# Performance work log

Hardware: AMD Instinct MI355X
Metric: run time of the kernel (lower is better)

The kernel has to match this reference:

```python
import jax, jax.numpy as jnp
import numpy as np
from jax import lax

TAU = 2.0
VTH = 1.0
EPS = 1e-5


def heaviside(x):
    return (x >= 0.0).astype(x.dtype)


def lif_scan(x):
    """x: [T, ...]; LIF with decay_input=True, v_reset=0 (hard reset)."""
    def step(v, xt):
        v = v + (xt - v) / TAU
        s = heaviside(v - VTH)
        v = v * (1.0 - s)
        return v, s
    _, out = lax.scan(step, jnp.zeros_like(x[0]), x)
    return out


def conv2d(x, w):
    return lax.conv_general_dilated(x, w, (1, 1), 'SAME',
                                    dimension_numbers=('NCHW', 'OIHW', 'NCHW'))


def bn(x, g, b, m, v):
    inv = lax.rsqrt(v + EPS)
    return (x - m[None, :, None, None]) * (g * inv)[None, :, None, None] + b[None, :, None, None]


def maxpool2(x):
    return lax.reduce_window(x, -jnp.inf, lax.max, (1, 1, 2, 2), (1, 1, 2, 2), 'VALID')


def conv_block(x, w, g, b, m, v, pool):
    T, B = x.shape[:2]
    y = x.reshape((T * B,) + x.shape[2:])
    y = bn(conv2d(y, w), g, b, m, v)
    y = y.reshape((T, B) + y.shape[1:])
    y = lif_scan(y)
    if pool:
        y = y.reshape((T * B,) + y.shape[2:])
        y = maxpool2(y)
        y = y.reshape((T, B) + y.shape[1:])
    return y


def setup_inputs() -> dict:
    key = jax.random.key(0)
    ks = jax.random.split(key, 12)
    x = jax.random.normal(ks[0], (8, 128, 3, 32, 32), jnp.float32)
    w1 = jax.random.normal(ks[1], (64, 3, 3, 3), jnp.float32) * 0.1
    w2 = jax.random.normal(ks[2], (128, 64, 3, 3), jnp.float32) * 0.05
    w3 = jax.random.normal(ks[3], (256, 128, 3, 3), jnp.float32) * 0.05
    fc1_w = jax.random.normal(ks[4], (512, 16384), jnp.float32) * 0.01
    raw = jax.random.normal(ks[5], (10, 512), jnp.float32)
    Q, _ = jnp.linalg.qr(raw.T)  # 10 <= 512: orthogonal prototypes
    protos = Q.T[:10]
    d = dict(x=x, w1=w1, w2=w2, w3=w3, fc1_w=fc1_w, protos=protos)
    for i, c in zip((1, 2, 3), (64, 128, 256)):
        d[f'g{i}'] = jnp.ones((c,), jnp.float32)
        d[f'b{i}'] = jnp.zeros((c,), jnp.float32)
        d[f'm{i}'] = jax.random.normal(jax.random.fold_in(key, 100 + i), (c,), jnp.float32) * 0.1
        d[f'var{i}'] = jax.random.uniform(jax.random.fold_in(key, 200 + i), (c,), jnp.float32) + 0.5
    return d


def reference(x, w1, g1, b1, m1, var1, w2, g2, b2, m2, var2,
              w3, g3, b3, m3, var3, fc1_w, protos):
    h = conv_block(x, w1, g1, b1, m1, var1, pool=False)   # [T,B,64,32,32]
    h = conv_block(h, w2, g2, b2, m2, var2, pool=True)    # [T,B,128,16,16]
    h = conv_block(h, w3, g3, b3, m3, var3, pool=True)    # [T,B,256,8,8]
    T, B = h.shape[:2]
    h = h.reshape(T, B, -1)                               # [T,B,16384]
    h = jnp.einsum('tbd,fd->tbf', h, fc1_w)
    h = lif_scan(h)                                        # [T,B,512]
    feat = h.mean(axis=0)                                  # [B,512]
    fn = feat / jnp.clip(jnp.linalg.norm(feat, axis=1, keepdims=True), 1e-12)
    pn = protos / jnp.clip(jnp.linalg.norm(protos, axis=1, keepdims=True), 1e-12)
    return fn @ pn.T * 10.0                                # [B,10]
```

## Files before the change

kernel.cpp:

```cpp
#include <hip/hip_runtime.h>
#include <stdint.h>

#define EPS 1e-5f

typedef __attribute__((ext_vector_type(4))) float f32x4;
typedef __attribute__((ext_vector_type(8))) __bf16 bf16x8;

__device__ __forceinline__ void gl_lds16(const void* g, void* l) {
    __builtin_amdgcn_global_load_lds(
        (const __attribute__((address_space(1))) void*)g,
        (__attribute__((address_space(3))) void*)l, 16, 0, 0);
}

__device__ __forceinline__ unsigned short f2bf(float f) {
    unsigned u = __builtin_bit_cast(unsigned, f);
    unsigned r = (u + 0x7FFFu + ((u >> 16) & 1u)) >> 16;
    return (unsigned short)r;
}
__device__ __forceinline__ float bf2f(unsigned short h) {
    unsigned u = ((unsigned)h) << 16;
    return __builtin_bit_cast(float, u);
}

#define OFF_W2S   0ULL
#define OFF_W3S   442368ULL
#define OFF_FCS   2211840ULL
#define OFF_S1M   52543488ULL
#define OFF_S2PM  60932096ULL
#define OFF_S3    65126400ULL
#define OFF_PRE4P 98680832ULL
#define OFF_FEAT  115458048ULL
#define OFF_PN    115720192ULL

__global__ void repack_w2s(const float* __restrict__ w2, unsigned short* __restrict__ out) {
    int i = blockIdx.x * 256 + threadIdx.x;
    if (i >= 73728) return;
    int oc = i / 576, rem = i % 576;
    int ic = rem / 9, tap = rem % 9;
    float w = w2[i];
    unsigned short hi = f2bf(w);  float r1 = w - bf2f(hi);
    unsigned short md = f2bf(r1); float r2 = r1 - bf2f(md);
    unsigned short lo = f2bf(r2);
    size_t base = ((size_t)(tap * 128 + oc)) * 64 + (((ic >> 3) ^ (oc & 7)) << 3) + (ic & 7);
    out[base] = hi; out[base + 73728] = md; out[base + 147456] = lo;
}
__global__ void repack_w3s(const float* __restrict__ w3, unsigned short* __restrict__ out) {
    int i = blockIdx.x * 256 + threadIdx.x;
    if (i >= 294912) return;
    int oc = i / 1152, rem = i % 1152;
    int ic = rem / 9, tap = rem % 9;
    float w = w3[i];
    unsigned short hi = f2bf(w);  float r1 = w - bf2f(hi);
    unsigned short md = f2bf(r1); float r2 = r1 - bf2f(md);
    unsigned short lo = f2bf(r2);
    int cc = tap * 2 + (ic >> 6), icl = ic & 63;
    size_t base = ((size_t)(cc * 256 + oc)) * 64 + (((icl >> 3) ^ (oc & 7)) << 3) + (icl & 7);
    out[base] = hi; out[base + 294912] = md; out[base + 589824] = lo;
}
__global__ void repack_fcs(const float* __restrict__ fw, unsigned short* __restrict__ out) {
    int i = blockIdx.x * 256 + threadIdx.x;
    if (i >= 8388608) return;
    int f = i >> 14, d = i & 16383;
    float w = fw[i];
    unsigned short hi = f2bf(w);  float r1 = w - bf2f(hi);
    unsigned short md = f2bf(r1); float r2 = r1 - bf2f(md);
    unsigned short lo = f2bf(r2);
    int cc = d >> 6, kl = d & 63;
    size_t base = (((size_t)cc << 9) + f) * 64 + (((kl >> 3) ^ (f & 7)) << 3) + (kl & 7);
    out[base] = hi; out[base + 8388608] = md; out[base + 16777216] = lo;
}

__global__ __launch_bounds__(256) void conv1_lif_pack(
    const float* __restrict__ x, const float* __restrict__ w1,
    const float* __restrict__ g1, const float* __restrict__ b1,
    const float* __restrict__ m1, const float* __restrict__ var1,
    unsigned long long* __restrict__ s1m)
{
    __shared__ float xt[3][3][40];
    int blk = blockIdx.x;
    int b = blk >> 5, y = blk & 31;
    int tid = threadIdx.x;
    int w = tid >> 6, lane = tid & 63;

    float wr[27];
#pragma unroll
    for (int j = 0; j < 27; ++j) wr[j] = w1[lane * 27 + j];
    float scale = g1[lane] / sqrtf(var1[lane] + EPS);
    float bias  = b1[lane] - m1[lane] * scale;

    float v[8];
#pragma unroll
    for (int p = 0; p < 8; ++p) v[p] = 0.f;

    for (int t = 0; t < 8; ++t) {
        __syncthreads();
        const float* xb = x + ((size_t)(t * 128 + b)) * 3072;
        for (int i = tid; i < 360; i += 256) {
            int ic = i / 120, rem = i % 120, dr = rem / 40, col = rem % 40;
            int yy = y + dr - 1, xx = col - 4;
            float val = 0.f;
            if (yy >= 0 && yy < 32 && xx >= 0 && xx < 32)
                val = xb[ic * 1024 + yy * 32 + xx];
            xt[ic][dr][col] = val;
        }
        __syncthreads();

        float acc[8];
#pragma unroll
        for (int p = 0; p < 8; ++p) acc[p] = 0.f;
#pragma unroll
        for (int ic = 0; ic < 3; ++ic)
#pragma unroll
        for (int dr = 0; dr < 3; ++dr) {
            const float* row = &xt[ic][dr][w * 8];
            float bf[16];
            *(float4*)&bf[0]  = *(const float4*)&row[0];
            *(float4*)&bf[4]  = *(const float4*)&row[4];
            *(float4*)&bf[8]  = *(const float4*)&row[8];
            *(float4*)&bf[12] = *(const float4*)&row[12];
#pragma unroll
            for (int p = 0; p < 8; ++p)
#pragma unroll
                for (int dxm = 0; dxm < 3; ++dxm)
                    acc[p] += bf[p + dxm + 3] * wr[ic * 9 + dr * 3 + dxm];
        }
        size_t base = ((size_t)t * 128 + b) * 1024 + y * 32 + w * 8;
#pragma unroll
        for (int p = 0; p < 8; ++p) {
            float pre = acc[p] * scale + bias;
            v[p] = v[p] + (pre - v[p]) * 0.5f;
            bool s = (v[p] >= 1.0f);
            unsigned long long mk = __ballot(s);
            if (s) v[p] = 0.f;
            if (lane == 0) s1m[base + p] = mk;
        }
    }
}

__global__ __launch_bounds__(256, 2) void conv2_mfma(
    const unsigned long long* __restrict__ s1m,
    const unsigned short* __restrict__ w2s,
    const float* __restrict__ g, const float* __restrict__ bb,
    const float* __restrict__ mm, const float* __restrict__ vv,
    unsigned long long* __restrict__ s2pm)
{
    __shared__ unsigned short A[128 * 64];
    __shared__ unsigned short B[3 * 128 * 64];
    __shared__ unsigned long long mt[6][34];
    __shared__ unsigned short pm16[2][16][8];

    int tid = threadIdx.x;
    int m0 = blockIdx.x << 7;
    int b = m0 >> 10;
    int pix0 = m0 & 1023;
    int y0 = pix0 >> 5;

    int w = tid >> 6, lane = tid & 63;
    int wm = w & 1, wn = w >> 1;
    int q = lane >> 4, r = lane & 15;
    int swr = r & 7;
    int am = tid >> 1, ah = tid & 1;
    int ay = am >> 5, ax = am & 31;
    int asw = am & 7;

    float scl[4], bia[4];
#pragma unroll
    for (int j = 0; j < 4; ++j) {
        int oc = wn * 64 + j * 16 + r;
        float s0 = g[oc] / sqrtf(vv[oc] + EPS);
        scl[j] = s0;
        bia[j] = bb[oc] - mm[oc] * s0;
    }

    float vr[4][4][4];
#pragma unroll
    for (int i = 0; i < 4; ++i)
#pragma unroll
        for (int j = 0; j < 4; ++j)
#pragma unroll
            for (int k = 0; k < 4; ++k) vr[i][j][k] = 0.f;

    const char* w2sb = (const char*)w2s;

    for (int t = 0; t < 8; ++t) {
        for (int i = tid; i < 204; i += 256) {
            int ly = i / 34, lx = i % 34;
            int yy = y0 + ly - 1, xx = lx - 1;
            unsigned long long mv = 0ULL;
            if (yy >= 0 && yy < 32 && xx >= 0 && xx < 32)
                mv = s1m[(size_t)t * 131072 + (b << 10) + (yy << 5) + xx];
            mt[ly][lx] = mv;
        }

        f32x4 acc[4][4];
#pragma unroll
        for (int i = 0; i < 4; ++i)
#pragma unroll
            for (int j = 0; j < 4; ++j) acc[i][j] = (f32x4){0.f, 0.f, 0.f, 0.f};

        for (int tap = 0; tap < 9; ++tap) {
            int dy = tap / 3, dx = tap - dy * 3;
            __syncthreads();
            {
                unsigned long long mk = mt[ay + dy][ax + dx];
                unsigned int wbits = (unsigned int)(mk >> (ah << 5));
#pragma unroll
                for (int c4 = 0; c4 < 4; ++c4) {
                    unsigned int bt = wbits >> (c4 << 3);
                    uint4 val;
                    val.x = ((bt & 1u) ? 0x3F80u : 0u)  | ((bt & 2u) ? 0x3F800000u : 0u);
                    val.y = ((bt & 4u) ? 0x3F80u : 0u)  | ((bt & 8u) ? 0x3F800000u : 0u);
                    val.z = ((bt & 16u) ? 0x3F80u : 0u) | ((bt & 32u) ? 0x3F800000u : 0u);
                    val.w = ((bt & 64u) ? 0x3F80u : 0u) | ((bt & 128u) ? 0x3F800000u : 0u);
                    int c = (ah << 2) + c4;
                    *(uint4*)((char*)A + am * 128 + ((c ^ asw) << 4)) = val;
                }
            }
            {
                const char* gb = w2sb + tap * 16384 + (w << 12) + (lane << 4);
                char* lb = (char*)B + (w << 12);
#pragma unroll
                for (int s = 0; s < 3; ++s)
#pragma unroll
                    for (int p = 0; p < 4; ++p)
                        gl_lds16(gb + s * 147456 + (p << 10), lb + s * 16384 + (p << 10));
            }
            __syncthreads();
#pragma unroll
            for (int ks = 0; ks < 2; ++ks) {
                bf16x8 af[4];
#pragma unroll
                for (int i = 0; i < 4; ++i)
                    af[i] = *(const bf16x8*)((const char*)A + (wm * 64 + i * 16 + r) * 128 + ((((ks << 2) + q) ^ swr) << 4));
#pragma unroll
                for (int s = 0; s < 3; ++s) {
                    bf16x8 bfr[4];
#pragma unroll
                    for (int j = 0; j < 4; ++j)
                        bfr[j] = *(const bf16x8*)((const char*)B + s * 16384 + (wn * 64 + j * 16 + r) * 128 + ((((ks << 2) + q) ^ swr) << 4));
#pragma unroll
                    for (int i = 0; i < 4; ++i)
#pragma unroll
                        for (int j = 0; j < 4; ++j)
                            acc[i][j] = __builtin_amdgcn_mfma_f32_16x16x32_bf16(af[i], bfr[j], acc[i][j], 0, 0, 0);
                }
            }
        }

        unsigned long long S = 0ULL;
#pragma unroll
        for (int i = 0; i < 4; ++i) {
#pragma unroll
            for (int j = 0; j < 4; ++j) {
#pragma unroll
                for (int reg = 0; reg < 4; ++reg) {
                    float pre = acc[i][j][reg] * scl[j] + bia[j];
                    float vo = vr[i][j][reg];
                    vo = vo + (pre - vo) * 0.5f;
                    bool sp = (vo >= 1.0f);
                    vr[i][j][reg] = sp ? 0.f : vo;
                    if (sp) S |= 1ULL << (i * 16 + j * 4 + reg);
                }
            }
        }
#pragma unroll
        for (int b1 = 0; b1 < 2; ++b1)
#pragma unroll
            for (int u = 0; u < 2; ++u)
#pragma unroll
                for (int j = 0; j < 4; ++j) {
                    int k0 = b1 * 16 + j * 4 + 2 * u;
                    bool sp = (((S >> k0) | (S >> (k0 + 1)) | (S >> (k0 + 32)) | (S >> (k0 + 33))) & 1ULL) != 0;
                    unsigned long long mk = __ballot(sp);
                    if (r == 0)
                        pm16[wm][b1 * 8 + (q << 1) + u][wn * 4 + j] = (unsigned short)(mk >> (q << 4));
                }
        __syncthreads();
        if (tid < 64) {
            int py = tid >> 5, px = (tid >> 1) & 15, h = tid & 1;
            unsigned long long vmk = *(unsigned long long*)&pm16[py][px][h << 2];
            s2pm[(size_t)t * 65536 + ((size_t)(b << 8) + ((y0 >> 1) + py) * 16 + px) * 2 + h] = vmk;
        }
    }
}

__global__ __launch_bounds__(256, 2) void conv3_mfma(
    const unsigned long long* __restrict__ s2pm,
    const unsigned short* __restrict__ w3s,
    const float* __restrict__ g, const float* __restrict__ bb,
    const float* __restrict__ mm, const float* __restrict__ vv,
    unsigned short* __restrict__ s3)
{
    __shared__ unsigned short A[128 * 64];
    __shared__ unsigned short B[3 * 128 * 64];
    __shared__ unsigned long long mt3[10][18][2];

    int tid = threadIdx.x;
    int m0 = blockIdx.x << 7;
    int n0 = blockIdx.y << 7;
    int b = m0 >> 8;
    int pix0 = m0 & 255;
    int y0 = pix0 >> 4;

    int w = tid >> 6, lane = tid & 63;
    int wm = w & 1, wn = w >> 1;
    int q = lane >> 4, r = lane & 15;
    int swr = r & 7;
    int am = tid >> 1, ah = tid & 1;
    int ay = am >> 4, ax = am & 15;
    int asw = am & 7;

    float scl[4], bia[4];
#pragma unroll
    for (int j = 0; j < 4; ++j) {
        int oc = n0 + wn * 64 + j * 16 + r;
        float s0 = g[oc] / sqrtf(vv[oc] + EPS);
        scl[j] = s0;
        bia[j] = bb[oc] - mm[oc] * s0;
    }

    float vr[4][4][4];
#pragma unroll
    for (int i = 0; i < 4; ++i)
#pragma unroll
        for (int j = 0; j < 4; ++j)
#pragma unroll
            for (int k = 0; k < 4; ++k) vr[i][j][k] = 0.f;

    const char* w3sb = (const char*)w3s;
    int bsw = b & 7;

    for (int t = 0; t < 8; ++t) {
        for (int i = tid; i < 180; i += 256) {
            int ly = i / 18, lx = i % 18;
            int yy = y0 + ly - 1, xx = lx - 1;
            unsigned long long v0 = 0ULL, v1 = 0ULL;
            if (yy >= 0 && yy < 16 && xx >= 0 && xx < 16) {
                const unsigned long long* p = &s2pm[(size_t)t * 65536 + ((size_t)(b << 8) + (yy << 4) + xx) * 2];
                v0 = p[0]; v1 = p[1];
            }
            mt3[ly][lx][0] = v0; mt3[ly][lx][1] = v1;
        }

        f32x4 acc[4][4];
#pragma unroll
        for (int i = 0; i < 4; ++i)
#pragma unroll
            for (int j = 0; j < 4; ++j) acc[i][j] = (f32x4){0.f, 0.f, 0.f, 0.f};

        for (int cc = 0; cc < 18; ++cc) {
            int tap = cc >> 1, h = cc & 1;
            int dy = tap / 3, dx = tap - dy * 3;
            __syncthreads();
            {
                unsigned long long mk = mt3[ay + dy][ax + dx][h];
                unsigned int wbits = (unsigned int)(mk >> (ah << 5));
#pragma unroll
                for (int c4 = 0; c4 < 4; ++c4) {
                    unsigned int bt = wbits >> (c4 << 3);
                    uint4 val;
                    val.x = ((bt & 1u) ? 0x3F80u : 0u)  | ((bt & 2u) ? 0x3F800000u : 0u);
                    val.y = ((bt & 4u) ? 0x3F80u : 0u)  | ((bt & 8u) ? 0x3F800000u : 0u);
                    val.z = ((bt & 16u) ? 0x3F80u : 0u) | ((bt & 32u) ? 0x3F800000u : 0u);
                    val.w = ((bt & 64u) ? 0x3F80u : 0u) | ((bt & 128u) ? 0x3F800000u : 0u);
                    int c = (ah << 2) + c4;
                    *(uint4*)((char*)A + am * 128 + ((c ^ asw) << 4)) = val;
                }
            }
            {
                const char* gb = w3sb + cc * 32768 + n0 * 128 + (w << 12) + (lane << 4);
                char* lb = (char*)B + (w << 12);
#pragma unroll
                for (int s = 0; s < 3; ++s)
#pragma unroll
                    for (int p = 0; p < 4; ++p)
                        gl_lds16(gb + s * 589824 + (p << 10), lb + s * 16384 + (p << 10));
            }
            __syncthreads();
#pragma unroll
            for (int ks = 0; ks < 2; ++ks) {
                bf16x8 af[4];
#pragma unroll
                for (int i = 0; i < 4; ++i)
                    af[i] = *(const bf16x8*)((const char*)A + (wm * 64 + i * 16 + r) * 128 + ((((ks << 2) + q) ^ swr) << 4));
#pragma unroll
                for (int s = 0; s < 3; ++s) {
                    bf16x8 bfr[4];
#pragma unroll
                    for (int j = 0; j < 4; ++j)
                        bfr[j] = *(const bf16x8*)((const char*)B + s * 16384 + (wn * 64 + j * 16 + r) * 128 + ((((ks << 2) + q) ^ swr) << 4));
#pragma unroll
                    for (int i = 0; i < 4; ++i)
#pragma unroll
                        for (int j = 0; j < 4; ++j)
                            acc[i][j] = __builtin_amdgcn_mfma_f32_16x16x32_bf16(af[i], bfr[j], acc[i][j], 0, 0, 0);
                }
            }
        }

        unsigned long long S = 0ULL;
#pragma unroll
        for (int i = 0; i < 4; ++i) {
#pragma unroll
            for (int j = 0; j < 4; ++j) {
#pragma unroll
                for (int reg = 0; reg < 4; ++reg) {
                    float pre = acc[i][j][reg] * scl[j] + bia[j];
                    float vo = vr[i][j][reg];
                    vo = vo + (pre - vo) * 0.5f;
                    bool sp = (vo >= 1.0f);
                    vr[i][j][reg] = sp ? 0.f : vo;
                    if (sp) S |= 1ULL << (i * 16 + j * 4 + reg);
                }
            }
        }
        unsigned short* s3t = s3 + (size_t)t * 2097152;
#pragma unroll
        for (int a2 = 0; a2 < 2; ++a2)
#pragma unroll
            for (int u = 0; u < 2; ++u)
#pragma unroll
                for (int j = 0; j < 4; ++j) {
                    int kA = 32 * a2 + j * 4 + 2 * u;
                    bool sp = (((S >> kA) | (S >> (kA + 1)) | (S >> (kA + 16)) | (S >> (kA + 17))) & 1ULL) != 0;
                    int oc = n0 + wn * 64 + j * 16 + r;
                    int y2 = (y0 >> 1) + wm * 2 + a2;
                    int x2 = (q << 1) + u;
                    s3t[(size_t)(b << 14) + oc * 64 + ((y2 ^ bsw) << 3) + x2] =
                        (unsigned short)(sp ? 0x3F80 : 0);
                }
    }
}

__global__ __launch_bounds__(256, 2) void fc_mfma(
    const unsigned short* __restrict__ s3,
    const unsigned short* __restrict__ fcs,
    float* __restrict__ pre4p)
{
    __shared__ unsigned short A[128 * 64];
    __shared__ unsigned short B[3 * 128 * 64];

    int tid = threadIdx.x;
    int m0 = blockIdx.x << 7;
    int n0 = blockIdx.y << 7;
    int kseg = blockIdx.z;
    int cc0 = kseg << 5;

    int w = tid >> 6, lane = tid & 63;
    int wm = w & 1, wn = w >> 1;
    int q = lane >> 4, r = lane & 15;
    int swr = r & 7;

    f32x4 acc[4][4];
#pragma unroll
    for (int i = 0; i < 4; ++i)
#pragma unroll
        for (int j = 0; j < 4; ++j) acc[i][j] = (f32x4){0.f, 0.f, 0.f, 0.f};

    const char* s3b = (const char*)s3;
    const char* fcsb = (const char*)fcs;

    for (int cc = cc0; cc < cc0 + 32; ++cc) {
        __syncthreads();
        {
            char* lb = (char*)A + (w << 12);
#pragma unroll
            for (int p = 0; p < 4; ++p)
                gl_lds16(s3b + (size_t)(m0 + w * 32 + p * 8 + (lane >> 3)) * 32768
                             + cc * 128 + ((lane & 7) << 4),
                         lb + (p << 10));
        }
        {
            const char* gb = fcsb + cc * 65536 + n0 * 128 + (w << 12) + (lane << 4);
            char* lb = (char*)B + (w << 12);
#pragma unroll
            for (int s = 0; s < 3; ++s)
#pragma unroll
                for (int p = 0; p < 4; ++p)
                    gl_lds16(gb + s * 16777216 + (p << 10), lb + s * 16384 + (p << 10));
        }
        __syncthreads();
#pragma unroll
        for (int ks = 0; ks < 2; ++ks) {
            bf16x8 af[4];
#pragma unroll
            for (int i = 0; i < 4; ++i)
                af[i] = *(const bf16x8*)((const char*)A + (wm * 64 + i * 16 + r) * 128 + ((((ks << 2) + q) ^ swr) << 4));
#pragma unroll
            for (int s = 0; s < 3; ++s) {
                bf16x8 bfr[4];
#pragma unroll
                for (int j = 0; j < 4; ++j)
                    bfr[j] = *(const bf16x8*)((const char*)B + s * 16384 + (wn * 64 + j * 16 + r) * 128 + ((((ks << 2) + q) ^ swr) << 4));
#pragma unroll
                for (int i = 0; i < 4; ++i)
#pragma unroll
                    for (int j = 0; j < 4; ++j)
                        acc[i][j] = __builtin_amdgcn_mfma_f32_16x16x32_bf16(af[i], bfr[j], acc[i][j], 0, 0, 0);
            }
        }
    }
#pragma unroll
    for (int i = 0; i < 4; ++i) {
#pragma unroll
        for (int j = 0; j < 4; ++j) {
            size_t base = ((size_t)kseg * 1024 + m0 + wm * 64 + i * 16 + (q << 2)) * 512
                        + n0 + wn * 64 + j * 16 + r;
#pragma unroll
            for (int reg = 0; reg < 4; ++reg)
                pre4p[base + (size_t)reg * 512] = acc[i][j][reg];
        }
    }
}

__global__ void lif4_mean(const float* __restrict__ P, float* __restrict__ feat) {
    int i = blockIdx.x * 256 + threadIdx.x;
    if (i >= 65536) return;
    int b = i >> 9, f = i & 511;
    float v = 0.f, sum = 0.f;
#pragma unroll
    for (int t = 0; t < 8; ++t) {
        float pre = 0.f;
#pragma unroll
        for (int s = 0; s < 8; ++s)
            pre += P[(size_t)s * 524288 + (size_t)(t * 128 + b) * 512 + f];
        v = v + (pre - v) * 0.5f;
        if (v >= 1.0f) { sum += 1.f; v = 0.f; }
    }
    feat[i] = sum * 0.125f;
}

__global__ void protos_norm(const float* __restrict__ P, float* __restrict__ pn) {
    int p = blockIdx.x;
    int lane = threadIdx.x;
    float ss = 0.f;
    for (int f = lane; f < 512; f += 64) { float x = P[p * 512 + f]; ss += x * x; }
#pragma unroll
    for (int o = 32; o > 0; o >>= 1) ss += __shfl_xor(ss, o);
    float inv = 1.f / fmaxf(sqrtf(ss), 1e-12f);
    for (int f = lane; f < 512; f += 64) pn[p * 512 + f] = P[p * 512 + f] * inv;
}

__global__ void final_logits(const float* __restrict__ feat, const float* __restrict__ pn,
                             float* __restrict__ out) {
    int b = blockIdx.x;
    int lane = threadIdx.x;
    float fr[8];
    float ss = 0.f;
#pragma unroll
    for (int j = 0; j < 8; ++j) { fr[j] = feat[b * 512 + j * 64 + lane]; ss += fr[j] * fr[j]; }
#pragma unroll
    for (int o = 32; o > 0; o >>= 1) ss += __shfl_xor(ss, o);
    float inv = 10.f / fmaxf(sqrtf(ss), 1e-12f);
    for (int p = 0; p < 10; ++p) {
        float d = 0.f;
#pragma unroll
        for (int j = 0; j < 8; ++j) d += fr[j] * pn[p * 512 + j * 64 + lane];
#pragma unroll
        for (int o = 32; o > 0; o >>= 1) d += __shfl_xor(d, o);
        if (lane == 0) out[b * 10 + p] = d * inv;
    }
}

extern "C" void kernel_launch(void* const* d_in, const int* in_sizes, int n_in,
                              void* d_out, int out_size, void* d_ws, size_t ws_size,
                              hipStream_t stream) {
    const float* x      = (const float*)d_in[0];
    const float* w1     = (const float*)d_in[1];
    const float* w2     = (const float*)d_in[2];
    const float* w3     = (const float*)d_in[3];
    const float* fc1    = (const float*)d_in[4];
    const float* protos = (const float*)d_in[5];
    const float* g1 = (const float*)d_in[6],  *b1 = (const float*)d_in[7];
    const float* m1 = (const float*)d_in[8],  *v1 = (const float*)d_in[9];
    const float* g2 = (const float*)d_in[10], *b2 = (const float*)d_in[11];
    const float* m2 = (const float*)d_in[12], *v2p = (const float*)d_in[13];
    const float* g3 = (const float*)d_in[14], *b3 = (const float*)d_in[15];
    const float* m3 = (const float*)d_in[16], *v3p = (const float*)d_in[17];

    char* ws = (char*)d_ws;
    unsigned short* w2s = (unsigned short*)(ws + OFF_W2S);
    unsigned short* w3s = (unsigned short*)(ws + OFF_W3S);
    unsigned short* fcs = (unsigned short*)(ws + OFF_FCS);
    unsigned long long* s1m  = (unsigned long long*)(ws + OFF_S1M);
    unsigned long long* s2pm = (unsigned long long*)(ws + OFF_S2PM);
    unsigned short* s3 = (unsigned short*)(ws + OFF_S3);
    float* pre4p = (float*)(ws + OFF_PRE4P);
    float* feat  = (float*)(ws + OFF_FEAT);
    float* pn    = (float*)(ws + OFF_PN);

    repack_w2s<<<288, 256, 0, stream>>>(w2, w2s);
    repack_w3s<<<1152, 256, 0, stream>>>(w3, w3s);
    repack_fcs<<<32768, 256, 0, stream>>>(fc1, fcs);

    conv1_lif_pack<<<4096, 256, 0, stream>>>(x, w1, g1, b1, m1, v1, s1m);
    conv2_mfma<<<1024, 256, 0, stream>>>(s1m, w2s, g2, b2, m2, v2p, s2pm);
    conv3_mfma<<<dim3(256, 2), 256, 0, stream>>>(s2pm, w3s, g3, b3, m3, v3p, s3);

    fc_mfma<<<dim3(8, 4, 8), 256, 0, stream>>>(s3, fcs, pre4p);
    lif4_mean<<<256, 256, 0, stream>>>(pre4p, feat);
    protos_norm<<<10, 64, 0, stream>>>(protos, pn);
    final_logits<<<128, 64, 0, stream>>>(feat, pn, (float*)d_out);
}
```

Baseline: 1.033 ms.

## Expand spike halo once per timestep and double-buffer weight slices in conv2/conv3

Conv2 and conv3 now expand the whole padded spike-mask halo into a bf16 LDS tile once per timestep (once per channel half in conv3). The old code re-expanded the A tile for every tap. Weight slices are streamed through a double-buffered LDS tile, so the next slice's global-to-LDS load overlaps the current MFMAs. The next timestep's mask is prefetched into a second mask buffer. This removes repeated expansion work and the two barriers per tap, but adds a barrier per weight slice, shrinks B staging, and changes LDS footprint and bank-access patterns.

```diff
diff --git a/kernel.cpp b/kernel.cpp
--- a/kernel.cpp
+++ b/kernel.cpp
@@ -20,6 +20,15 @@
 __device__ __forceinline__ float bf2f(unsigned short h) {
     unsigned u = ((unsigned)h) << 16;
     return __builtin_bit_cast(float, u);
+}
+
+__device__ __forceinline__ uint4 expand8(unsigned int bt) {
+    uint4 val;
+    val.x = ((bt & 1u) ? 0x3F80u : 0u)  | ((bt & 2u) ? 0x3F800000u : 0u);
+    val.y = ((bt & 4u) ? 0x3F80u : 0u)  | ((bt & 8u) ? 0x3F800000u : 0u);
+    val.z = ((bt & 16u) ? 0x3F80u : 0u) | ((bt & 32u) ? 0x3F800000u : 0u);
+    val.w = ((bt & 64u) ? 0x3F80u : 0u) | ((bt & 128u) ? 0x3F800000u : 0u);
+    return val;
 }
 
 #define OFF_W2S   0ULL
@@ -144,9 +153,9 @@
     const float* __restrict__ mm, const float* __restrict__ vv,
     unsigned long long* __restrict__ s2pm)
 {
-    __shared__ unsigned short A[128 * 64];
-    __shared__ unsigned short B[3 * 128 * 64];
-    __shared__ unsigned long long mt[6][34];
+    __shared__ unsigned long long mt[2][6][34];
+    __shared__ unsigned short Aexp[204 * 64];
+    __shared__ unsigned short Bt[2][8192];
     __shared__ unsigned short pm16[2][16][8];
 
     int tid = threadIdx.x;
@@ -159,9 +168,13 @@
     int wm = w & 1, wn = w >> 1;
     int q = lane >> 4, r = lane & 15;
     int swr = r & 7;
-    int am = tid >> 1, ah = tid & 1;
-    int ay = am >> 5, ax = am & 31;
-    int asw = am & 7;
+
+    int yloc[4], xloc[4];
+#pragma unroll
+    for (int i = 0; i < 4; ++i) {
+        int mrow = wm * 64 + i * 16 + r;
+        yloc[i] = mrow >> 5; xloc[i] = mrow & 31;
+    }
 
     float scl[4], bia[4];
 #pragma unroll
@@ -182,15 +195,49 @@
 
     const char* w2sb = (const char*)w2s;
 
+    for (int i = tid; i < 204; i += 256) {
+        int ly = i / 34, lx = i % 34;
+        int yy = y0 + ly - 1, xx = lx - 1;
+        unsigned long long mv = 0ULL;
+        if (yy >= 0 && yy < 32 && xx >= 0 && xx < 32)
+            mv = s1m[(b << 10) + (yy << 5) + xx];
+        mt[0][ly][lx] = mv;
+    }
+    {
+        const char* gb = w2sb + (w << 12) + (lane << 4);
+        char* lb = (char*)Bt[0] + (w << 12);
+#pragma unroll
+        for (int p = 0; p < 4; ++p) gl_lds16(gb + (p << 10), lb + (p << 10));
+    }
+    __syncthreads();
+
+    int it = 0;
     for (int t = 0; t < 8; ++t) {
-        for (int i = tid; i < 204; i += 256) {
-            int ly = i / 34, lx = i % 34;
-            int yy = y0 + ly - 1, xx = lx - 1;
-            unsigned long long mv = 0ULL;
-            if (yy >= 0 && yy < 32 && xx >= 0 && xx < 32)
-                mv = s1m[(size_t)t * 131072 + (b << 10) + (yy << 5) + xx];
-            mt[ly][lx] = mv;
-        }
+        {
+            const unsigned long long* mtc = &mt[t & 1][0][0];
+            for (int u = tid; u < 408; u += 256) {
+                int p = u >> 1, hc = u & 1;
+                unsigned long long mk = mtc[p];
+                unsigned int w32 = (unsigned int)(mk >> (hc << 5));
+#pragma unroll
+                for (int c4 = 0; c4 < 4; ++c4) {
+                    int c = (hc << 2) + c4;
+                    *(uint4*)((char*)Aexp + p * 128 + ((c ^ (p & 7)) << 4)) =
+                        expand8(w32 >> (c4 << 3));
+                }
+            }
+        }
+        if (t < 7) {
+            for (int i = tid; i < 204; i += 256) {
+                int ly = i / 34, lx = i % 34;
+                int yy = y0 + ly - 1, xx = lx - 1;
+                unsigned long long mv = 0ULL;
+                if (yy >= 0 && yy < 32 && xx >= 0 && xx < 32)
+                    mv = s1m[(size_t)(t + 1) * 131072 + (b << 10) + (yy << 5) + xx];
+                mt[(t + 1) & 1][ly][lx] = mv;
+            }
+        }
+        __syncthreads();
 
         f32x4 acc[4][4];
 #pragma unroll
@@ -200,58 +247,48 @@
 
         for (int tap = 0; tap < 9; ++tap) {
             int dy = tap / 3, dx = tap - dy * 3;
-            __syncthreads();
-            {
-                unsigned long long mk = mt[ay + dy][ax + dx];
-                unsigned int wbits = (unsigned int)(mk >> (ah << 5));
-#pragma unroll
-                for (int c4 = 0; c4 < 4; ++c4) {
-                    unsigned int bt = wbits >> (c4 << 3);
-                    uint4 val;
-                    val.x = ((bt & 1u) ? 0x3F80u : 0u)  | ((bt & 2u) ? 0x3F800000u : 0u);
-                    val.y = ((bt & 4u) ? 0x3F80u : 0u)  | ((bt & 8u) ? 0x3F800000u : 0u);
-                    val.z = ((bt & 16u) ? 0x3F80u : 0u) | ((bt & 32u) ? 0x3F800000u : 0u);
-                    val.w = ((bt & 64u) ? 0x3F80u : 0u) | ((bt & 128u) ? 0x3F800000u : 0u);
-                    int c = (ah << 2) + c4;
-                    *(uint4*)((char*)A + am * 128 + ((c ^ asw) << 4)) = val;
-                }
-            }
-            {
-                const char* gb = w2sb + tap * 16384 + (w << 12) + (lane << 4);
-                char* lb = (char*)B + (w << 12);
-#pragma unroll
-                for (int s = 0; s < 3; ++s)
-#pragma unroll
-                    for (int p = 0; p < 4; ++p)
-                        gl_lds16(gb + s * 147456 + (p << 10), lb + s * 16384 + (p << 10));
-            }
-            __syncthreads();
-#pragma unroll
-            for (int ks = 0; ks < 2; ++ks) {
-                bf16x8 af[4];
-#pragma unroll
-                for (int i = 0; i < 4; ++i)
-                    af[i] = *(const bf16x8*)((const char*)A + (wm * 64 + i * 16 + r) * 128 + ((((ks << 2) + q) ^ swr) << 4));
-#pragma unroll
-                for (int s = 0; s < 3; ++s) {
+            bf16x8 af[4][2];
+#pragma unroll
+            for (int i = 0; i < 4; ++i) {
+                int p = (yloc[i] + dy) * 34 + xloc[i] + dx;
+                const char* base = (const char*)Aexp + p * 128;
+                int sw = p & 7;
+                af[i][0] = *(const bf16x8*)(base + ((q ^ sw) << 4));
+                af[i][1] = *(const bf16x8*)(base + (((4 + q) ^ sw) << 4));
+            }
+#pragma unroll
+            for (int s = 0; s < 3; ++s) {
+                {
+                    int s2 = s + 1, tap2 = tap;
+                    if (s2 == 3) { s2 = 0; tap2 = tap + 1; if (tap2 == 9) tap2 = 0; }
+                    const char* gb = w2sb + s2 * 147456 + tap2 * 16384 + (w << 12) + (lane << 4);
+                    char* lb = (char*)Bt[(it + 1) & 1] + (w << 12);
+#pragma unroll
+                    for (int p = 0; p < 4; ++p) gl_lds16(gb + (p << 10), lb + (p << 10));
+                }
+                const char* Bc = (const char*)Bt[it & 1];
+#pragma unroll
+                for (int ks = 0; ks < 2; ++ks) {
                     bf16x8 bfr[4];
 #pragma unroll
                     for (int j = 0; j < 4; ++j)
-                        bfr[j] = *(const bf16x8*)((const char*)B + s * 16384 + (wn * 64 + j * 16 + r) * 128 + ((((ks << 2) + q) ^ swr) << 4));
+                        bfr[j] = *(const bf16x8*)(Bc + (wn * 64 + j * 16 + r) * 128 + ((((ks << 2) + q) ^ swr) << 4));
 #pragma unroll
                     for (int i = 0; i < 4; ++i)
 #pragma unroll
                         for (int j = 0; j < 4; ++j)
-                            acc[i][j] = __builtin_amdgcn_mfma_f32_16x16x32_bf16(af[i], bfr[j], acc[i][j], 0, 0, 0);
-                }
+                            acc[i][j] = __builtin_amdgcn_mfma_f32_16x16x32_bf16(af[i][ks], bfr[j], acc[i][j], 0, 0, 0);
+                }
+                __syncthreads();
+                ++it;
             }
         }
 
         unsigned long long S = 0ULL;
 #pragma unroll
-        for (int i = 0; i < 4; ++i) {
-#pragma unroll
-            for (int j = 0; j < 4; ++j) {
+        for (int i = 0; i < 4; ++i)
+#pragma unroll
+            for (int j = 0; j < 4; ++j)
 #pragma unroll
                 for (int reg = 0; reg < 4; ++reg) {
                     float pre = acc[i][j][reg] * scl[j] + bia[j];
@@ -261,8 +298,6 @@
                     vr[i][j][reg] = sp ? 0.f : vo;
                     if (sp) S |= 1ULL << (i * 16 + j * 4 + reg);
                 }
-            }
-        }
 #pragma unroll
         for (int b1 = 0; b1 < 2; ++b1)
 #pragma unroll
@@ -291,9 +326,9 @@
     const float* __restrict__ mm, const float* __restrict__ vv,
     unsigned short* __restrict__ s3)
 {
-    __shared__ unsigned short A[128 * 64];
-    __shared__ unsigned short B[3 * 128 * 64];
-    __shared__ unsigned long long mt3[10][18][2];
+    __shared__ unsigned long long mt3[2][10][18][2];
+    __shared__ unsigned short Aexp[180 * 64];
+    __shared__ unsigned short Bt[2][8192];
 
     int tid = threadIdx.x;
     int m0 = blockIdx.x << 7;
@@ -306,9 +341,13 @@
     int wm = w & 1, wn = w >> 1;
     int q = lane >> 4, r = lane & 15;
     int swr = r & 7;
-    int am = tid >> 1, ah = tid & 1;
-    int ay = am >> 4, ax = am & 15;
-    int asw = am & 7;
+
+    int yloc[4], xloc[4];
+#pragma unroll
+    for (int i = 0; i < 4; ++i) {
+        int mrow = wm * 64 + i * 16 + r;
+        yloc[i] = mrow >> 4; xloc[i] = mrow & 15;
+    }
 
     float scl[4], bia[4];
 #pragma unroll
@@ -330,17 +369,53 @@
     const char* w3sb = (const char*)w3s;
     int bsw = b & 7;
 
+    for (int i = tid; i < 180; i += 256) {
+        int ly = i / 18, lx = i % 18;
+        int yy = y0 + ly - 1, xx = lx - 1;
+        unsigned long long v0 = 0ULL, v1 = 0ULL;
+        if (yy >= 0 && yy < 16 && xx >= 0 && xx < 16) {
+            const unsigned long long* p = &s2pm[((size_t)(b << 8) + (yy << 4) + xx) * 2];
+            v0 = p[0]; v1 = p[1];
+        }
+        mt3[0][ly][lx][0] = v0; mt3[0][ly][lx][1] = v1;
+    }
+    {
+        const char* gb = w3sb + n0 * 128 + (w << 12) + (lane << 4);
+        char* lb = (char*)Bt[0] + (w << 12);
+#pragma unroll
+        for (int p = 0; p < 4; ++p) gl_lds16(gb + (p << 10), lb + (p << 10));
+    }
+    __syncthreads();
+
+    int it = 0;
     for (int t = 0; t < 8; ++t) {
-        for (int i = tid; i < 180; i += 256) {
-            int ly = i / 18, lx = i % 18;
-            int yy = y0 + ly - 1, xx = lx - 1;
-            unsigned long long v0 = 0ULL, v1 = 0ULL;
-            if (yy >= 0 && yy < 16 && xx >= 0 && xx < 16) {
-                const unsigned long long* p = &s2pm[(size_t)t * 65536 + ((size_t)(b << 8) + (yy << 4) + xx) * 2];
-                v0 = p[0]; v1 = p[1];
-            }
-            mt3[ly][lx][0] = v0; mt3[ly][lx][1] = v1;
-        }
+        {
+            const unsigned long long* mtc = &mt3[t & 1][0][0][0];
+            for (int u = tid; u < 360; u += 256) {
+                int p = u >> 1, hc = u & 1;
+                unsigned long long mk = mtc[p * 2];
+                unsigned int w32 = (unsigned int)(mk >> (hc << 5));
+#pragma unroll
+                for (int c4 = 0; c4 < 4; ++c4) {
+                    int c = (hc << 2) + c4;
+                    *(uint4*)((char*)Aexp + p * 128 + ((c ^ (p & 7)) << 4)) =
+                        expand8(w32 >> (c4 << 3));
+                }
+            }
+        }
+        if (t < 7) {
+            for (int i = tid; i < 180; i += 256) {
+                int ly = i / 18, lx = i % 18;
+                int yy = y0 + ly - 1, xx = lx - 1;
+                unsigned long long v0 = 0ULL, v1 = 0ULL;
+                if (yy >= 0 && yy < 16 && xx >= 0 && xx < 16) {
+                    const unsigned long long* p = &s2pm[(size_t)(t + 1) * 65536 + ((size_t)(b << 8) + (yy << 4) + xx) * 2];
+                    v0 = p[0]; v1 = p[1];
+                }
+                mt3[(t + 1) & 1][ly][lx][0] = v0; mt3[(t + 1) & 1][ly][lx][1] = v1;
+            }
+        }
+        __syncthreads();
 
         f32x4 acc[4][4];
 #pragma unroll
@@ -348,61 +423,71 @@
 #pragma unroll
             for (int j = 0; j < 4; ++j) acc[i][j] = (f32x4){0.f, 0.f, 0.f, 0.f};
 
-        for (int cc = 0; cc < 18; ++cc) {
-            int tap = cc >> 1, h = cc & 1;
-            int dy = tap / 3, dx = tap - dy * 3;
-            __syncthreads();
-            {
-                unsigned long long mk = mt3[ay + dy][ax + dx][h];
-                unsigned int wbits = (unsigned int)(mk >> (ah << 5));
-#pragma unroll
-                for (int c4 = 0; c4 < 4; ++c4) {
-                    unsigned int bt = wbits >> (c4 << 3);
-                    uint4 val;
-                    val.x = ((bt & 1u) ? 0x3F80u : 0u)  | ((bt & 2u) ? 0x3F800000u : 0u);
-                    val.y = ((bt & 4u) ? 0x3F80u : 0u)  | ((bt & 8u) ? 0x3F800000u : 0u);
-                    val.z = ((bt & 16u) ? 0x3F80u : 0u) | ((bt & 32u) ? 0x3F800000u : 0u);
-                    val.w = ((bt & 64u) ? 0x3F80u : 0u) | ((bt & 128u) ? 0x3F800000u : 0u);
-                    int c = (ah << 2) + c4;
-                    *(uint4*)((char*)A + am * 128 + ((c ^ asw) << 4)) = val;
-                }
-            }
-            {
-                const char* gb = w3sb + cc * 32768 + n0 * 128 + (w << 12) + (lane << 4);
-                char* lb = (char*)B + (w << 12);
-#pragma unroll
-                for (int s = 0; s < 3; ++s)
-#pragma unroll
-                    for (int p = 0; p < 4; ++p)
-                        gl_lds16(gb + s * 589824 + (p << 10), lb + s * 16384 + (p << 10));
-            }
-            __syncthreads();
-#pragma unroll
-            for (int ks = 0; ks < 2; ++ks) {
-                bf16x8 af[4];
-#pragma unroll
-                for (int i = 0; i < 4; ++i)
-                    af[i] = *(const bf16x8*)((const char*)A + (wm * 64 + i * 16 + r) * 128 + ((((ks << 2) + q) ^ swr) << 4));
+        for (int h = 0; h < 2; ++h) {
+            for (int tap = 0; tap < 9; ++tap) {
+                int dy = tap / 3, dx = tap - dy * 3;
+                int cc = tap * 2 + h;
+                bf16x8 af[4][2];
+#pragma unroll
+                for (int i = 0; i < 4; ++i) {
+                    int p = (yloc[i] + dy) * 18 + xloc[i] + dx;
+                    const char* base = (const char*)Aexp + p * 128;
+                    int sw = p & 7;
+                    af[i][0] = *(const bf16x8*)(base + ((q ^ sw) << 4));
+                    af[i][1] = *(const bf16x8*)(base + (((4 + q) ^ sw) << 4));
+                }
 #pragma unroll
                 for (int s = 0; s < 3; ++s) {
-                    bf16x8 bfr[4];
-#pragma unroll
-                    for (int j = 0; j < 4; ++j)
-                        bfr[j] = *(const bf16x8*)((const char*)B + s * 16384 + (wn * 64 + j * 16 + r) * 128 + ((((ks << 2) + q) ^ swr) << 4));
-#pragma unroll
-                    for (int i = 0; i < 4; ++i)
+                    {
+                        int s2 = s + 1, cc2 = cc;
+                        if (s2 == 3) {
+                            s2 = 0; cc2 = cc + 2;
+                            if (cc2 >= 18) cc2 = (h == 0) ? 1 : 0;
+                        }
+                        const char* gb = w3sb + s2 * 589824 + cc2 * 32768 + n0 * 128 + (w << 12) + (lane << 4);
+                        char* lb = (char*)Bt[(it + 1) & 1] + (w << 12);
+#pragma unroll
+                        for (int p = 0; p < 4; ++p) gl_lds16(gb + (p << 10), lb + (p << 10));
+                    }
+                    const char* Bc = (const char*)Bt[it & 1];
+#pragma unroll
+                    for (int ks = 0; ks < 2; ++ks) {
+                        bf16x8 bfr[4];
 #pragma unroll
                         for (int j = 0; j < 4; ++j)
-                            acc[i][j] = __builtin_amdgcn_mfma_f32_16x16x32_bf16(af[i], bfr[j], acc[i][j], 0, 0, 0);
-                }
+                            bfr[j] = *(const bf16x8*)(Bc + (wn * 64 + j * 16 + r) * 128 + ((((ks << 2) + q) ^ swr) << 4));
+#pragma unroll
+                        for (int i = 0; i < 4; ++i)
+#pragma unroll
+                            for (int j = 0; j < 4; ++j)
+                                acc[i][j] = __builtin_amdgcn_mfma_f32_16x16x32_bf16(af[i][ks], bfr[j], acc[i][j], 0, 0, 0);
+                    }
+                    __syncthreads();
+                    ++it;
+                }
+            }
+            if (h == 0) {
+                const unsigned long long* mtc = &mt3[t & 1][0][0][0];
+                for (int u = tid; u < 360; u += 256) {
+                    int p = u >> 1, hc = u & 1;
+                    unsigned long long mk = mtc[p * 2 + 1];
+                    unsigned int w32 = (unsigned int)(mk >> (hc << 5));
+#pragma unroll
+                    for (int c4 = 0; c4 < 4; ++c4) {
+                        int c = (hc << 2) + c4;
+                        *(uint4*)((char*)Aexp + p * 128 + ((c ^ (p & 7)) << 4)) =
+                            expand8(w32 >> (c4 << 3));
+                    }
+                }
+                __syncthreads();
             }
         }
 
         unsigned long long S = 0ULL;
 #pragma unroll
-        for (int i = 0; i < 4; ++i) {
-#pragma unroll
-            for (int j = 0; j < 4; ++j) {
+        for (int i = 0; i < 4; ++i)
+#pragma unroll
+            for (int j = 0; j < 4; ++j)
 #pragma unroll
                 for (int reg = 0; reg < 4; ++reg) {
                     float pre = acc[i][j][reg] * scl[j] + bia[j];
@@ -412,8 +497,6 @@
                     vr[i][j][reg] = sp ? 0.f : vo;
                     if (sp) S |= 1ULL << (i * 16 + j * 4 + reg);
                 }
-            }
-        }
         unsigned short* s3t = s3 + (size_t)t * 2097152;
 #pragma unroll
         for (int a2 = 0; a2 < 2; ++a2)
```

Result: slower. 1.127 ms (+9.0%).
